# Performance work log

Measured on AMD Instinct MI355X. Metric: run time of the kernel, lower is better.

## Reference

```python
import jax, jax.numpy as jnp
import numpy as np

EMBED_DIM = 2048
NUM_HEADS = 16
HEAD_DIM = EMBED_DIM // NUM_HEADS  # 128


def setup_inputs() -> dict:
    key = jax.random.key(0)
    ks = jax.random.split(key, 11)
    B, S, D, Hd = 2, 2048, EMBED_DIM, HEAD_DIM
    s_in = 1.0 / np.sqrt(D)
    return {
        "query": jax.random.normal(ks[0], (B, S, D), dtype=jnp.float32),
        "key": jax.random.normal(ks[1], (B, S, D), dtype=jnp.float32),
        "value": jax.random.normal(ks[2], (B, S, D), dtype=jnp.float32),
        "Wq": jax.random.normal(ks[3], (D, D), dtype=jnp.float32) * s_in,
        "bq": jax.random.normal(ks[4], (D,), dtype=jnp.float32) * s_in,
        "Wk": jax.random.normal(ks[5], (D, Hd), dtype=jnp.float32) * s_in,
        "bk": jax.random.normal(ks[6], (Hd,), dtype=jnp.float32) * s_in,
        "Wv": jax.random.normal(ks[7], (D, Hd), dtype=jnp.float32) * s_in,
        "bv": jax.random.normal(ks[8], (Hd,), dtype=jnp.float32) * s_in,
        "Wo": jax.random.normal(ks[9], (D, D), dtype=jnp.float32) * s_in,
        "bo": jax.random.normal(ks[10], (D,), dtype=jnp.float32) * s_in,
    }


def reference(query, key, value, Wq, bq, Wk, bk, Wv, bv, Wo, bo):
    B, S, D = query.shape
    H, Hd = NUM_HEADS, HEAD_DIM
    # projections
    Q = (query @ Wq + bq).reshape(B, S, H, Hd).transpose(0, 2, 1, 3)  # [B,H,S,Hd]
    K = key @ Wk + bk    # [B,S,Hd] single shared KV head
    V = value @ Wv + bv  # [B,S,Hd]
    scale = 1.0 / jnp.sqrt(jnp.asarray(Hd, dtype=Q.dtype))
    # MQA: broadcast single K/V head across H query heads
    scores = jnp.einsum("bhsd,btd->bhst", Q, K) * scale  # [B,H,S,S]
    attn = jax.nn.softmax(scores, axis=-1)
    out = jnp.einsum("bhst,btd->bhsd", attn, V)  # [B,H,S,Hd]
    out = out.transpose(0, 2, 1, 3).reshape(B, S, D)
    return out @ Wo + bo
```

## Files before the change

### kernel.cpp

```cpp
#include <hip/hip_runtime.h>
#include <stdint.h>

#define S_LEN 2048
#define EMBED 2048
#define NHEADS 16
#define HDIM 128

typedef __attribute__((ext_vector_type(8))) short bf16x8;
typedef __attribute__((ext_vector_type(4))) float f32x4;
typedef unsigned short us;

static __device__ __forceinline__ us f2b(float f) {
    union { float f; unsigned u; } x; x.f = f;
    unsigned r = x.u + 0x7fffu + ((x.u >> 16) & 1u);
    return (us)(r >> 16);
}

static __device__ __forceinline__ unsigned cvtpk(float a, float b) {
    unsigned r;
    asm("v_cvt_pk_bf16_f32 %0, %1, %2" : "=v"(r) : "v"(a), "v"(b));
    return r;
}

static __device__ __forceinline__ uint2 pack4(float a, float b, float c, float d) {
    uint2 u;
    u.x = cvtpk(a, b);
    u.y = cvtpk(c, d);
    return u;
}

static __device__ __forceinline__ float fexp2(float x) {
    float r;
    asm("v_exp_f32 %0, %1" : "=v"(r) : "v"(x));
    return r;
}

static __device__ __forceinline__ void gl_lds16(const void* g, void* l) {
    __builtin_amdgcn_global_load_lds(
        (const __attribute__((address_space(1))) void*)g,
        (__attribute__((address_space(3))) void*)l, 16, 0, 0);
}


static __device__ __forceinline__ void dma_tile(const us* __restrict__ g, int k0,
                                                us* dst, int tid) {
#pragma unroll
    for (int i = 0; i < 4; i++) {
        int sl = i * 256 + tid;
        int row = sl >> 3, cp = sl & 7, c = cp ^ (row & 7);
        gl_lds16(g + (size_t)row * 2048 + k0 + c * 8,
                 (char*)dst + (i * 256 + (tid & 192)) * 16);
    }
}

static __device__ __forceinline__ void loadA_f32(const float* __restrict__ g,
                                                 float4 pf[8]) {
#pragma unroll
    for (int i = 0; i < 8; i++) pf[i] = ((const float4*)g)[i];
}

static __device__ __forceinline__ void writeA_f32(us* dst, const float4 pf[8],
                                                  int row, int h) {
#pragma unroll
    for (int cc = 0; cc < 4; cc++) {
        int p = (h * 4 + cc) ^ (row & 7);
        float4 a = pf[cc * 2], b = pf[cc * 2 + 1];
        uint4 u;
        u.x = (unsigned)f2b(a.x) | ((unsigned)f2b(a.y) << 16);
        u.y = (unsigned)f2b(a.z) | ((unsigned)f2b(a.w) << 16);
        u.z = (unsigned)f2b(b.x) | ((unsigned)f2b(b.y) << 16);
        u.w = (unsigned)f2b(b.z) | ((unsigned)f2b(b.w) << 16);
        *(uint4*)&dst[row * 64 + p * 8] = u;
    }
}

static __device__ __forceinline__ void frag_mfma(const us* curA, const us* curB,
                                                 int wm, int wn, int lm, int quad,
                                                 f32x4 acc[4][4]) {
#pragma unroll
    for (int kc = 0; kc < 2; kc++) {
        bf16x8 af[4], bfr[4];
#pragma unroll
        for (int mi = 0; mi < 4; mi++) {
            int row = wm * 64 + mi * 16 + lm;
            int p = (kc * 4 + quad) ^ (row & 7);
            af[mi] = *(const bf16x8*)&curA[row * 64 + p * 8];
        }
#pragma unroll
        for (int ni = 0; ni < 4; ni++) {
            int row = wn * 64 + ni * 16 + lm;
            int p = (kc * 4 + quad) ^ (row & 7);
            bfr[ni] = *(const bf16x8*)&curB[row * 64 + p * 8];
        }
#pragma unroll
        for (int mi = 0; mi < 4; mi++)
#pragma unroll
            for (int ni = 0; ni < 4; ni++)
                acc[mi][ni] = __builtin_amdgcn_mfma_f32_16x16x32_bf16(
                    af[mi], bfr[ni], acc[mi][ni], 0, 0, 0);
    }
}

__global__ void tcast3(const float* __restrict__ Wq, const float* __restrict__ Wk,
                       const float* __restrict__ Wv, const float* __restrict__ query,
                       us* __restrict__ Wqt, us* __restrict__ Wkvt,
                       us* __restrict__ qbf) {
    int b = blockIdx.x;
    if (b >= 2304) {
        int id = (b - 2304) * 256 + threadIdx.x;
        const float4* in4 = (const float4*)query;
        float4 a = in4[id * 2], c = in4[id * 2 + 1];
        uint4 u;
        u.x = (unsigned)f2b(a.x) | ((unsigned)f2b(a.y) << 16);
        u.y = (unsigned)f2b(a.z) | ((unsigned)f2b(a.w) << 16);
        u.z = (unsigned)f2b(c.x) | ((unsigned)f2b(c.y) << 16);
        u.w = (unsigned)f2b(c.z) | ((unsigned)f2b(c.w) << 16);
        ((uint4*)qbf)[id] = u;
        return;
    }
    const float* in; us* out; int N, rel;
    if (b < 2048)      { in = Wq; out = Wqt;  N = 2048; rel = b; }
    else if (b < 2176) { in = Wk; out = Wkvt; N = 128;  rel = b - 2048; }
    else               { in = Wv; out = Wkvt + (size_t)128 * 2048; N = 128; rel = b - 2176; }
    int id = rel * 256 + threadIdx.x;
    int n = id & (N - 1), k0 = (id / N) * 8;
    us t8[8];
#pragma unroll
    for (int j = 0; j < 8; j++) t8[j] = f2b(in[(size_t)(k0 + j) * N + n]);
    *(uint4*)&out[(size_t)n * 2048 + k0] = *(uint4*)t8;
}

__global__ __launch_bounds__(256, 2) void proj_qkv(
    const float* __restrict__ key, const float* __restrict__ value,
    const us* __restrict__ qbf, const us* __restrict__ Wqt,
    const us* __restrict__ Wkvt, const float* __restrict__ bq,
    us* __restrict__ Qh, float* __restrict__ part)
{
    __shared__ __align__(16) us A0[128 * 64], A1[128 * 64];
    __shared__ __align__(16) us B0[128 * 64], B1[128 * 64];

    const int tid = threadIdx.x;
    const int lane = tid & 63, w = tid >> 6, lm = lane & 15, quad = lane >> 4;
    const int wm = w >> 1, wn = w & 1;
    const int id = blockIdx.x;

    f32x4 acc[4][4];
#pragma unroll
    for (int i = 0; i < 4; i++)
#pragma unroll
        for (int j = 0; j < 4; j++) acc[i][j] = (f32x4){0.f, 0.f, 0.f, 0.f};

    if (id < 512) {
        const int bn = (id & 15) * 128, bm = (id >> 4) * 128;
        const us* Atile = qbf + (size_t)bm * 2048;
        const us* Btile = Wqt + (size_t)bn * 2048;

        dma_tile(Atile, 0, A0, tid);
        dma_tile(Btile, 0, B0, tid);

        for (int kk = 0; kk < 32; kk += 2) {
            __syncthreads();
            if (kk + 1 < 32) { dma_tile(Atile, (kk + 1) * 64, A1, tid);
                               dma_tile(Btile, (kk + 1) * 64, B1, tid); }
            frag_mfma(A0, B0, wm, wn, lm, quad, acc);
            __syncthreads();
            if (kk + 2 < 32) { dma_tile(Atile, (kk + 2) * 64, A0, tid);
                               dma_tile(Btile, (kk + 2) * 64, B0, tid); }
            frag_mfma(A1, B1, wm, wn, lm, quad, acc);
        }

#pragma unroll
        for (int mi = 0; mi < 4; mi++)
#pragma unroll
            for (int ni = 0; ni < 4; ni++) {
                int col = bn + wn * 64 + ni * 16 + lm;
                float bv = bq[col];
#pragma unroll
                for (int r = 0; r < 4; r++) {
                    int row = bm + wm * 64 + mi * 16 + quad * 4 + r;
                    float v = acc[mi][ni][r] + bv;
                    int b = row >> 11, s = row & 2047;
                    int hh = col >> 7, hd = col & 127;
                    size_t addr = (((size_t)(b * 16 + hh) * 2048 + s) << 7)
                                  + (((hd >> 3) ^ (s & 7)) << 3) + (hd & 7);
                    Qh[addr] = f2b(v);
                }
            }
    } else {
        int e = id - 512;
        int z = e >> 6, r = e & 63, isV = r & 1;
        int bm = (r >> 1) * 128, bn = isV * 128;
        const float* Atile = (isV ? value : key) + (size_t)bm * 2048;
        const us* Btile = Wkvt + (size_t)bn * 2048;
        const int kbeg = z * 512, iters = 8;
        const int arow = tid >> 1, h = tid & 1;
        const float* Ag = Atile + (size_t)arow * 2048 + h * 32;

        float4 pf[8];
        loadA_f32(Ag + kbeg, pf);
        dma_tile(Btile, kbeg, B0, tid);
        writeA_f32(A0, pf, arow, h);

        for (int kk = 0; kk < iters; kk += 2) {
            const int k1 = kbeg + (kk + 1) * 64;
            const int k2 = kbeg + (kk + 2) * 64;
            __syncthreads();
            if (kk + 1 < iters) { loadA_f32(Ag + k1, pf); dma_tile(Btile, k1, B1, tid); }
            frag_mfma(A0, B0, wm, wn, lm, quad, acc);
            if (kk + 1 < iters) writeA_f32(A1, pf, arow, h);
            __syncthreads();
            if (kk + 2 < iters) { loadA_f32(Ag + k2, pf); dma_tile(Btile, k2, B0, tid); }
            frag_mfma(A1, B1, wm, wn, lm, quad, acc);
            if (kk + 2 < iters) writeA_f32(A0, pf, arow, h);
        }

        float* pp = part + (size_t)z * 1048576;
#pragma unroll
        for (int mi = 0; mi < 4; mi++)
#pragma unroll
            for (int ni = 0; ni < 4; ni++) {
                int col = bn + wn * 64 + ni * 16 + lm;
#pragma unroll
                for (int r = 0; r < 4; r++) {
                    int row = bm + wm * 64 + mi * 16 + quad * 4 + r;
                    pp[(size_t)row * 256 + col] = acc[mi][ni][r];
                }
            }
    }
}

__global__ void finish_wot(const float* __restrict__ part, const float* __restrict__ bk,
                           const float* __restrict__ bv, us* __restrict__ Kb,
                           us* __restrict__ Vt, const float* __restrict__ Wo,
                           us* __restrict__ Wot) {
    int b = blockIdx.x;
    if (b < 2048) {
        int id = b * 256 + threadIdx.x;
        int n = id & 2047, k0 = (id >> 11) * 8;
        us t8[8];
#pragma unroll
        for (int j = 0; j < 8; j++) t8[j] = f2b(Wo[(size_t)(k0 + j) * 2048 + n]);
        *(uint4*)&Wot[(size_t)n * 2048 + k0] = *(uint4*)t8;
    } else {
        int id = (b - 2048) * 256 + threadIdx.x;
        int row = id >> 8, n = id & 255;
        float s = part[id] + part[1048576 + id] + part[2097152 + id] + part[3145728 + id];
        int bb = row >> 11, t = row & 2047;
        if (n < 128) {
            int hd = n;
            s += bk[hd];
            Kb[((size_t)(bb * 2048 + t) << 7) + (((hd >> 3) ^ (t & 7)) << 3) + (hd & 7)] = f2b(s);
        } else {
            int hd = n - 128;
            s += bv[hd];
            size_t addr = (((size_t)(bb * 64 + (t >> 5)) * 128 + hd) << 5)
                          + ((((t >> 3) & 3) ^ ((hd >> 1) & 3)) << 3) + (t & 7);
            Vt[addr] = f2b(s);
        }
    }
}

__global__ __launch_bounds__(256, 2) void mqa_attn(
    const us* __restrict__ Qh, const us* __restrict__ Kb,
    const us* __restrict__ Vt, us* __restrict__ AO)
{
    __shared__ __align__(16) char smem[65536];
    us* Qs  = (us*)smem;
    us* Ps  = (us*)smem;
    us* Ksb = (us*)(smem + 32768);
    us* Vts = (us*)(smem + 49152);
    float* Lb = (float*)(smem + 32768);

    const int tid  = threadIdx.x;
    const int lane = tid & 63;
    const int w    = tid >> 6;
    const int lm   = lane & 15;
    const int quad = lane >> 4;
    const int wm = w >> 1, wn = w & 1;
    const int q0 = blockIdx.x * 128;
    const int h  = blockIdx.y;
    const int b  = blockIdx.z;
    const float C = 0.12751743150179665f;

    const us* Qtile = Qh + (((size_t)(b * 16 + h) * 2048 + q0) << 7);
    const us* Kbase = Kb + ((size_t)b * 2048 << 7);
    const us* Vbase = Vt + (size_t)b * 64 * 4096;

#pragma unroll
    for (int i = 0; i < 8; i++) {
        int sl = w * 512 + i * 64 + lane;
        gl_lds16(Qtile + sl * 8, smem + (w * 512 + i * 64) * 16);
    }
#pragma unroll
    for (int i = 0; i < 2; i++) {
        int sl = w * 128 + i * 64 + lane;
        gl_lds16(Kbase + sl * 8, (char*)Ksb + (w * 128 + i * 64) * 16);
        gl_lds16(Vbase + sl * 8, (char*)Vts + (w * 128 + i * 64) * 16);
    }
    __syncthreads();

    bf16x8 qf[4][4];
#pragma unroll
    for (int nt = 0; nt < 4; nt++)
#pragma unroll
        for (int ks = 0; ks < 4; ks++) {
            int q = wn * 64 + nt * 16 + lm;
            int cp = (ks * 4 + quad) ^ (q & 7);
            qf[nt][ks] = *(const bf16x8*)&Qs[q * 128 + cp * 8];
        }
    __syncthreads();

    f32x4 oacc[4][4];
#pragma unroll
    for (int i = 0; i < 4; i++)
#pragma unroll
        for (int j = 0; j < 4; j++) oacc[i][j] = (f32x4){0.f, 0.f, 0.f, 0.f};
    float lsum[4] = {0.f, 0.f, 0.f, 0.f};

    for (int it = 0; it < 64; ++it) {
        const int p = it & 1;
        const us* Kst = Ksb + p * 4096;

        if (it < 63) {
            const us* kg = Kbase + (it + 1) * 4096;
#pragma unroll
            for (int i = 0; i < 2; i++) {
                int sl = w * 128 + i * 64 + lane;
                gl_lds16(kg + sl * 8, (char*)Ksb + (1 - p) * 8192 + (w * 128 + i * 64) * 16);
            }
        }

        f32x4 sacc[4];
#pragma unroll
        for (int nt = 0; nt < 4; nt++) sacc[nt] = (f32x4){0.f, 0.f, 0.f, 0.f};
        __builtin_amdgcn_s_setprio(1);
#pragma unroll
        for (int ks = 0; ks < 4; ks++) {
            int t = wm * 16 + lm;
            int cp = (ks * 4 + quad) ^ (lm & 7);
            bf16x8 kf = *(const bf16x8*)&Kst[t * 128 + cp * 8];
#pragma unroll
            for (int nt = 0; nt < 4; nt++)
                sacc[nt] = __builtin_amdgcn_mfma_f32_16x16x32_bf16(
                    kf, qf[nt][ks], sacc[nt], 0, 0, 0);
        }
        __builtin_amdgcn_s_setprio(0);

        us* Pw = Ps + p * 4096;
#pragma unroll
        for (int nt = 0; nt < 4; nt++) {
            int q = wn * 64 + nt * 16 + lm;
            float p0 = fexp2(sacc[nt][0] * C);
            float p1 = fexp2(sacc[nt][1] * C);
            float p2 = fexp2(sacc[nt][2] * C);
            float p3 = fexp2(sacc[nt][3] * C);
            lsum[nt] += (p0 + p1) + (p2 + p3);
            int tb = wm * 16 + quad * 4;
            int cp = (tb >> 3) ^ ((q >> 1) & 3);
            *(uint2*)&Pw[q * 32 + cp * 8 + (tb & 7)] = pack4(p0, p1, p2, p3);
        }

        __syncthreads();

        const us* Vst = Vts + p * 4096;
        const us* Pr = Ps + p * 4096;
        bf16x8 vf[4], pfr[4];
#pragma unroll
        for (int mt = 0; mt < 4; mt++) {
            int hd = (wm * 4 + mt) * 16 + lm;
            int cp = quad ^ ((hd >> 1) & 3);
            vf[mt] = *(const bf16x8*)&Vst[hd * 32 + cp * 8];
        }
#pragma unroll
        for (int nt = 0; nt < 4; nt++) {
            int q = (wn * 4 + nt) * 16 + lm;
            int cp = quad ^ ((q >> 1) & 3);
            pfr[nt] = *(const bf16x8*)&Pr[q * 32 + cp * 8];
        }
        __builtin_amdgcn_s_setprio(1);
#pragma unroll
        for (int mt = 0; mt < 4; mt++)
#pragma unroll
            for (int nt = 0; nt < 4; nt++)
                oacc[mt][nt] = __builtin_amdgcn_mfma_f32_16x16x32_bf16(
                    vf[mt], pfr[nt], oacc[mt][nt], 0, 0, 0);
        __builtin_amdgcn_s_setprio(0);

        if (it < 63) {
            const us* vg = Vbase + (it + 1) * 4096;
#pragma unroll
            for (int i = 0; i < 2; i++) {
                int sl = w * 128 + i * 64 + lane;
                gl_lds16(vg + sl * 8, (char*)Vts + (1 - p) * 8192 + (w * 128 + i * 64) * 16);
            }
        }
    }

#pragma unroll
    for (int nt = 0; nt < 4; nt++) {
        lsum[nt] += __shfl_xor(lsum[nt], 16);
        lsum[nt] += __shfl_xor(lsum[nt], 32);
    }
    if (quad == 0) {
#pragma unroll
        for (int nt = 0; nt < 4; nt++)
            Lb[wm * 128 + wn * 64 + nt * 16 + lm] = lsum[nt];
    }
    __syncthreads();

#pragma unroll
    for (int nt = 0; nt < 4; nt++) {
        int q = (wn * 4 + nt) * 16 + lm;
        float linv = 1.f / (Lb[q] + Lb[128 + q]);
#pragma unroll
        for (int mt = 0; mt < 4; mt++) {
            int hdb = (wm * 4 + mt) * 16 + quad * 4;
            uint2 u = pack4(oacc[mt][nt][0] * linv, oacc[mt][nt][1] * linv,
                            oacc[mt][nt][2] * linv, oacc[mt][nt][3] * linv);
            *(uint2*)&AO[((size_t)(b * 2048 + q0 + q)) * 2048 + h * 128 + hdb] = u;
        }
    }
}

__global__ __launch_bounds__(256, 2) void oproj(
    const us* __restrict__ AO, const us* __restrict__ Wot,
    const float* __restrict__ bo, float* __restrict__ out)
{
    __shared__ __align__(16) us A0[128 * 64], A1[128 * 64];
    __shared__ __align__(16) us B0[128 * 64], B1[128 * 64];

    const int tid = threadIdx.x;
    const int lane = tid & 63, w = tid >> 6, lm = lane & 15, quad = lane >> 4;
    const int wm = w >> 1, wn = w & 1;
    const int bn = blockIdx.x * 128, bm = blockIdx.y * 128;
    const us* Atile = AO + (size_t)bm * 2048;
    const us* Btile = Wot + (size_t)bn * 2048;

    f32x4 acc[4][4];
#pragma unroll
    for (int i = 0; i < 4; i++)
#pragma unroll
        for (int j = 0; j < 4; j++) acc[i][j] = (f32x4){0.f, 0.f, 0.f, 0.f};

    dma_tile(Atile, 0, A0, tid);
    dma_tile(Btile, 0, B0, tid);

    for (int kk = 0; kk < 32; kk += 2) {
        __syncthreads();
        if (kk + 1 < 32) { dma_tile(Atile, (kk + 1) * 64, A1, tid);
                           dma_tile(Btile, (kk + 1) * 64, B1, tid); }
        frag_mfma(A0, B0, wm, wn, lm, quad, acc);
        __syncthreads();
        if (kk + 2 < 32) { dma_tile(Atile, (kk + 2) * 64, A0, tid);
                           dma_tile(Btile, (kk + 2) * 64, B0, tid); }
        frag_mfma(A1, B1, wm, wn, lm, quad, acc);
    }

#pragma unroll
    for (int mi = 0; mi < 4; mi++)
#pragma unroll
        for (int ni = 0; ni < 4; ni++) {
            int col = bn + wn * 64 + ni * 16 + lm;
            float bv = bo[col];
#pragma unroll
            for (int r = 0; r < 4; r++) {
                int row = bm + wm * 64 + mi * 16 + quad * 4 + r;
                out[(size_t)row * 2048 + col] = acc[mi][ni][r] + bv;
            }
        }
}

extern "C" void kernel_launch(void* const* d_in, const int* in_sizes, int n_in,
                              void* d_out, int out_size, void* d_ws, size_t ws_size,
                              hipStream_t stream) {
    const float* query = (const float*)d_in[0];
    const float* key   = (const float*)d_in[1];
    const float* value = (const float*)d_in[2];
    const float* Wq = (const float*)d_in[3];
    const float* bq = (const float*)d_in[4];
    const float* Wk = (const float*)d_in[5];
    const float* bk = (const float*)d_in[6];
    const float* Wv = (const float*)d_in[7];
    const float* bv = (const float*)d_in[8];
    const float* Wo = (const float*)d_in[9];
    const float* bo = (const float*)d_in[10];
    float* out = (float*)d_out;

    char* ws = (char*)d_ws;
    us*    Wqt  = (us*)ws;
    us*    Wot  = Wqt;
    us*    Wkvt = (us*)(ws + 8388608);
    us*    Qh   = (us*)(ws + 9437184);
    float* part = (float*)(ws + 26214400);
    us*    AO   = (us*)part;
    us*    Kb   = (us*)(ws + 42991616);
    us*    Vtb  = (us*)(ws + 44040192);
    us*    qbf  = (us*)(ws + 45088768);

    dim3 blk(256);
    tcast3<<<6400, blk, 0, stream>>>(Wq, Wk, Wv, query, Wqt, Wkvt, qbf);
    proj_qkv<<<768, blk, 0, stream>>>(key, value, qbf, Wqt, Wkvt, bq, Qh, part);
    finish_wot<<<6144, blk, 0, stream>>>(part, bk, bv, Kb, Vtb, Wo, Wot);
    mqa_attn<<<dim3(16, 16, 2), blk, 0, stream>>>(Qh, Kb, Vtb, AO);
    oproj<<<dim3(16, 32), blk, 0, stream>>>(AO, Wot, bo, out);
}
```

Baseline: 336.6 us.

## Load Q and K fragments directly to registers, fold softmax scale into Q projection

The attention kernel no longer stages Q and K in shared memory. Q fragments are read straight from global memory, and K fragments are register double-buffered with global prefetch of the next tile, which cuts LDS from 64KB to about 33KB and may allow more resident blocks. The softmax scale constant is folded into the Q projection epilogue before bf16 rounding, removing a multiply per score. The V prefetch is moved earlier, before the PV MFMAs. In exchange, K loads now go through global/L2 per wave with redundant reads across waves, and the extra registers may raise register pressure.

New measurement: 333.4 us. Within noise of the previous version (-1.0%).

```diff
diff --git a/kernel.cpp b/kernel.cpp
--- a/kernel.cpp
+++ b/kernel.cpp
@@ -143,6 +143,7 @@
     const int lane = tid & 63, w = tid >> 6, lm = lane & 15, quad = lane >> 4;
     const int wm = w >> 1, wn = w & 1;
     const int id = blockIdx.x;
+    const float CQ = 0.12751743150179665f;
 
     f32x4 acc[4][4];
 #pragma unroll
@@ -178,7 +179,7 @@
 #pragma unroll
                 for (int r = 0; r < 4; r++) {
                     int row = bm + wm * 64 + mi * 16 + quad * 4 + r;
-                    float v = acc[mi][ni][r] + bv;
+                    float v = (acc[mi][ni][r] + bv) * CQ;
                     int b = row >> 11, s = row & 2047;
                     int hh = col >> 7, hd = col & 127;
                     size_t addr = (((size_t)(b * 16 + hh) * 2048 + s) << 7)
@@ -264,11 +265,9 @@
     const us* __restrict__ Qh, const us* __restrict__ Kb,
     const us* __restrict__ Vt, us* __restrict__ AO)
 {
-    __shared__ __align__(16) char smem[65536];
-    us* Qs  = (us*)smem;
+    __shared__ __align__(16) char smem[33792];
     us* Ps  = (us*)smem;
-    us* Ksb = (us*)(smem + 32768);
-    us* Vts = (us*)(smem + 49152);
+    us* Vts = (us*)(smem + 16384);
     float* Lb = (float*)(smem + 32768);
 
     const int tid  = threadIdx.x;
@@ -280,24 +279,16 @@
     const int q0 = blockIdx.x * 128;
     const int h  = blockIdx.y;
     const int b  = blockIdx.z;
-    const float C = 0.12751743150179665f;
 
     const us* Qtile = Qh + (((size_t)(b * 16 + h) * 2048 + q0) << 7);
     const us* Kbase = Kb + ((size_t)b * 2048 << 7);
     const us* Vbase = Vt + (size_t)b * 64 * 4096;
 
 #pragma unroll
-    for (int i = 0; i < 8; i++) {
-        int sl = w * 512 + i * 64 + lane;
-        gl_lds16(Qtile + sl * 8, smem + (w * 512 + i * 64) * 16);
-    }
-#pragma unroll
     for (int i = 0; i < 2; i++) {
         int sl = w * 128 + i * 64 + lane;
-        gl_lds16(Kbase + sl * 8, (char*)Ksb + (w * 128 + i * 64) * 16);
         gl_lds16(Vbase + sl * 8, (char*)Vts + (w * 128 + i * 64) * 16);
     }
-    __syncthreads();
 
     bf16x8 qf[4][4];
 #pragma unroll
@@ -306,8 +297,17 @@
         for (int ks = 0; ks < 4; ks++) {
             int q = wn * 64 + nt * 16 + lm;
             int cp = (ks * 4 + quad) ^ (q & 7);
-            qf[nt][ks] = *(const bf16x8*)&Qs[q * 128 + cp * 8];
-        }
+            qf[nt][ks] = *(const bf16x8*)&Qtile[q * 128 + cp * 8];
+        }
+
+    const int trow = wm * 16 + lm;
+    bf16x8 kfc[4], kfn[4];
+#pragma unroll
+    for (int ks = 0; ks < 4; ks++) {
+        int cp = (ks * 4 + quad) ^ (lm & 7);
+        kfc[ks] = *(const bf16x8*)&Kbase[(size_t)trow * 128 + cp * 8];
+    }
+
     __syncthreads();
 
     f32x4 oacc[4][4];
@@ -319,14 +319,13 @@
 
     for (int it = 0; it < 64; ++it) {
         const int p = it & 1;
-        const us* Kst = Ksb + p * 4096;
 
         if (it < 63) {
-            const us* kg = Kbase + (it + 1) * 4096;
-#pragma unroll
-            for (int i = 0; i < 2; i++) {
-                int sl = w * 128 + i * 64 + lane;
-                gl_lds16(kg + sl * 8, (char*)Ksb + (1 - p) * 8192 + (w * 128 + i * 64) * 16);
+            const us* kg = Kbase + (size_t)(it + 1) * 4096 + (size_t)trow * 128;
+#pragma unroll
+            for (int ks = 0; ks < 4; ks++) {
+                int cp = (ks * 4 + quad) ^ (lm & 7);
+                kfn[ks] = *(const bf16x8*)&kg[cp * 8];
             }
         }
 
@@ -336,13 +335,10 @@
         __builtin_amdgcn_s_setprio(1);
 #pragma unroll
         for (int ks = 0; ks < 4; ks++) {
-            int t = wm * 16 + lm;
-            int cp = (ks * 4 + quad) ^ (lm & 7);
-            bf16x8 kf = *(const bf16x8*)&Kst[t * 128 + cp * 8];
 #pragma unroll
             for (int nt = 0; nt < 4; nt++)
                 sacc[nt] = __builtin_amdgcn_mfma_f32_16x16x32_bf16(
-                    kf, qf[nt][ks], sacc[nt], 0, 0, 0);
+                    kfc[ks], qf[nt][ks], sacc[nt], 0, 0, 0);
         }
         __builtin_amdgcn_s_setprio(0);
 
@@ -350,10 +346,10 @@
 #pragma unroll
         for (int nt = 0; nt < 4; nt++) {
             int q = wn * 64 + nt * 16 + lm;
-            float p0 = fexp2(sacc[nt][0] * C);
-            float p1 = fexp2(sacc[nt][1] * C);
-            float p2 = fexp2(sacc[nt][2] * C);
-            float p3 = fexp2(sacc[nt][3] * C);
+            float p0 = fexp2(sacc[nt][0]);
+            float p1 = fexp2(sacc[nt][1]);
+            float p2 = fexp2(sacc[nt][2]);
+            float p3 = fexp2(sacc[nt][3]);
             lsum[nt] += (p0 + p1) + (p2 + p3);
             int tb = wm * 16 + quad * 4;
             int cp = (tb >> 3) ^ ((q >> 1) & 3);
@@ -362,6 +358,15 @@
 
         __syncthreads();
 
+        if (it < 63) {
+            const us* vg = Vbase + (it + 1) * 4096;
+#pragma unroll
+            for (int i = 0; i < 2; i++) {
+                int sl = w * 128 + i * 64 + lane;
+                gl_lds16(vg + sl * 8, (char*)Vts + (1 - p) * 8192 + (w * 128 + i * 64) * 16);
+            }
+        }
+
         const us* Vst = Vts + p * 4096;
         const us* Pr = Ps + p * 4096;
         bf16x8 vf[4], pfr[4];
@@ -386,14 +391,8 @@
                     vf[mt], pfr[nt], oacc[mt][nt], 0, 0, 0);
         __builtin_amdgcn_s_setprio(0);
 
-        if (it < 63) {
-            const us* vg = Vbase + (it + 1) * 4096;
-#pragma unroll
-            for (int i = 0; i < 2; i++) {
-                int sl = w * 128 + i * 64 + lane;
-                gl_lds16(vg + sl * 8, (char*)Vts + (1 - p) * 8192 + (w * 128 + i * 64) * 16);
-            }
-        }
+#pragma unroll
+        for (int ks = 0; ks < 4; ks++) kfc[ks] = kfn[ks];
     }
 
 #pragma unroll
```
